# Performance work log

Hardware: AMD Instinct MI355X
Metric: run time of the kernel (lower is better)

The kernel has to match this reference:

```python
import jax, jax.numpy as jnp
import numpy as np
from jax import lax

NUM_HEADS = 8
EMBED_DIM = 256
KEY_DIM = EMBED_DIM // NUM_HEADS  # 32


def rotate_every_two(x):
    x1 = x[..., ::2]
    x2 = x[..., 1::2]
    return jnp.stack((-x2, x1), axis=-1).reshape(x.shape)


def theta_shift(x, sin, cos):
    return x * cos + rotate_every_two(x) * sin


def setup_inputs() -> dict:
    key = jax.random.key(0)
    ks = jax.random.split(key, 16)
    b, H, W, E = 16, 64, 64, EMBED_DIM
    kd = KEY_DIM
    gain = 2 ** (-2.5)
    std_proj = gain * (2.0 / (E + E)) ** 0.5  # xavier_normal with gain
    std_out = (2.0 / (E + E)) ** 0.5
    return {
        "x": jax.random.normal(ks[0], (b, H, W, E), jnp.float32),
        "sin": jax.random.normal(ks[1], (H, W, kd), jnp.float32),
        "cos": jax.random.normal(ks[2], (H, W, kd), jnp.float32),
        "mask_h": jax.random.normal(ks[3], (NUM_HEADS, H, H), jnp.float32),
        "mask_w": jax.random.normal(ks[4], (NUM_HEADS, W, W), jnp.float32),
        "q_w": jax.random.normal(ks[5], (E, E), jnp.float32) * std_proj,
        "q_b": jnp.zeros((E,), jnp.float32),
        "k_w": jax.random.normal(ks[6], (E, E), jnp.float32) * std_proj,
        "k_b": jnp.zeros((E,), jnp.float32),
        "v_w": jax.random.normal(ks[7], (E, E), jnp.float32) * std_proj,
        "v_b": jnp.zeros((E,), jnp.float32),
        "lepe_w": jax.random.normal(ks[8], (5, 5, 1, E), jnp.float32) * 0.05,  # HWIO depthwise
        "lepe_b": jnp.zeros((E,), jnp.float32),
        "out_w": jax.random.normal(ks[9], (E, E), jnp.float32) * std_out,
        "out_b": jnp.zeros((E,), jnp.float32),
    }


def reference(x, sin, cos, mask_h, mask_w, q_w, q_b, k_w, k_b, v_w, v_b,
              lepe_w, lepe_b, out_w, out_b):
    b, H, W, E = x.shape
    nH, kd = NUM_HEADS, KEY_DIM
    vd = E // nH
    scaling = kd ** (-0.5)

    q = x @ q_w + q_b                       # [b,H,W,E]
    k = (x @ k_w + k_b) * scaling
    v = x @ v_w + v_b

    # depthwise 5x5 conv (lepe), NHWC
    lepe = lax.conv_general_dilated(
        v, lepe_w, window_strides=(1, 1), padding=[(2, 2), (2, 2)],
        dimension_numbers=("NHWC", "HWIO", "NHWC"), feature_group_count=E) + lepe_b

    q = q.reshape(b, H, W, nH, kd)
    k = k.reshape(b, H, W, nH, kd)
    v = v.reshape(b, H, W, nH, vd)

    sin_b = sin[:, :, None, :]              # [H,W,1,kd]
    cos_b = cos[:, :, None, :]
    qr = theta_shift(q, sin_b, cos_b)       # [b,H,W,nH,kd]
    kr = theta_shift(k, sin_b, cos_b)

    # width-wise attention: scores [b,H,nH,W,W]
    qk_w = jnp.einsum("bhqnd,bhknd->bhnqk", qr, kr)
    attn_w = jax.nn.softmax(qk_w + mask_w[None, None], axis=-1)
    v1 = jnp.einsum("bhnqk,bhknd->bhqnd", attn_w, v)  # [b,H,W,nH,vd]

    # height-wise attention: scores [b,W,nH,H,H]
    qk_h = jnp.einsum("bqwnd,bkwnd->bwnqk", qr, kr)
    attn_h = jax.nn.softmax(qk_h + mask_h[None, None], axis=-1)
    out = jnp.einsum("bwnqk,bkwnd->bqwnd", attn_h, v1)  # [b,H,W,nH,vd]

    out = out.reshape(b, H, W, E) + lepe
    return out @ out_w + out_b
```

## Files before the change

### kernel.cpp

```cpp
#include <hip/hip_runtime.h>

typedef unsigned short u16;
typedef __attribute__((ext_vector_type(4))) float f32x4;
typedef __attribute__((ext_vector_type(8))) short bf16x8;
typedef __attribute__((ext_vector_type(8))) u16 u16x8;
typedef __attribute__((ext_vector_type(4))) u16 u16x4v;

#define DI __device__ __forceinline__

DI u16 f2bf(float f) {
  unsigned int x = __float_as_uint(f);
  unsigned int r = (x + 0x7fffu + ((x >> 16) & 1u)) >> 16;
  return (u16)r;
}
DI float bf2f(u16 u) { return __uint_as_float(((unsigned int)u) << 16); }

__global__ __launch_bounds__(256) void pack_kernel(
    const float* __restrict__ qw, const float* __restrict__ qb,
    const float* __restrict__ kw, const float* __restrict__ kb,
    const float* __restrict__ vw, const float* __restrict__ vb,
    const float* __restrict__ ow,
    u16* __restrict__ wqkvT, float* __restrict__ bias, u16* __restrict__ owT)
{
  const int r = blockIdx.x;
  const int t = threadIdx.x;
  if (r < 768) {
    const int p = r >> 8, c = r & 255;
    const float* wsrc = p == 0 ? qw : (p == 1 ? kw : vw);
    const float sc = (p == 1) ? 0.17677669529663687f : 1.0f;
    wqkvT[r * 256 + t] = f2bf(wsrc[t * 256 + c] * sc);
    if (t == 0) {
      const float* bs = p == 0 ? qb : (p == 1 ? kb : vb);
      bias[r] = bs[c] * sc;
    }
  } else {
    const int c = r - 768;
    owT[c * 256 + t] = f2bf(ow[t * 256 + c]);
  }
}

__global__ __launch_bounds__(256) void convert_kernel(
    const float* __restrict__ x, u16* __restrict__ xb)
{
  const int idx = blockIdx.x * 256 + threadIdx.x;
  const int tile = idx >> 12;
  const int within = idx & 4095;
  const int r = within >> 5;
  const int bc = (within & 31) << 4;
  const int sbc = bc ^ ((r & 7) << 4);
  const int row = (tile << 7) + r;
  const float* sp = x + row * 256 + (sbc >> 1);
  const float4 a = *reinterpret_cast<const float4*>(sp);
  const float4 b = *reinterpret_cast<const float4*>(sp + 4);
  u16x8 o;
  o[0] = f2bf(a.x); o[1] = f2bf(a.y); o[2] = f2bf(a.z); o[3] = f2bf(a.w);
  o[4] = f2bf(b.x); o[5] = f2bf(b.y); o[6] = f2bf(b.z); o[7] = f2bf(b.w);
  *reinterpret_cast<u16x8*>(xb + (idx << 3)) = o;
}

__global__ __launch_bounds__(256, 2) void qkv_gemm_kernel(
    const u16* __restrict__ xb, const u16* __restrict__ wT, const float* __restrict__ bias,
    const float* __restrict__ sinp, const float* __restrict__ cosp,
    u16* __restrict__ qr, u16* __restrict__ kr, u16* __restrict__ v)
{
  __shared__ u16 As[32768];
  __shared__ float Tr[4][1024];
  const int t = threadIdx.x;
  const int wave = t >> 6, lane = t & 63;
  const int g = lane >> 4, lr = lane & 15;
  const int wr = wave >> 1, wc = wave & 1;
  const int m0 = blockIdx.x * 128;

  {
    const u16* src = xb + (size_t)blockIdx.x * 32768;
    auto gsrc = (const __attribute__((address_space(1))) u16*)src;
    auto lds = (__attribute__((address_space(3))) u16*)As;
#pragma unroll
    for (int i = 0; i < 16; ++i) {
      const int o = wave * 8192 + i * 512;
      __builtin_amdgcn_global_load_lds(
          (const __attribute__((address_space(1))) void*)(gsrc + o + lane * 8),
          (__attribute__((address_space(3))) void*)(lds + o), 16, 0, 0);
    }
  }
  __syncthreads();

  const char* Ab = (const char*)As;
  float* Trw = Tr[wave];
  const int tl = (lane >> 3);
  const int cg8 = (lane & 7) * 8;

  for (int cg = 0; cg < 6; ++cg) {
    const int c0 = cg * 128;
    f32x4 acc[4][4];
#pragma unroll
    for (int i = 0; i < 4; ++i)
#pragma unroll
      for (int j = 0; j < 4; ++j) acc[i][j] = (f32x4){0.f, 0.f, 0.f, 0.f};

#pragma unroll
    for (int ks = 0; ks < 8; ++ks) {
      bf16x8 af[4], bfr[4];
#pragma unroll
      for (int mt = 0; mt < 4; ++mt) {
        const int rr = wr * 64 + mt * 16 + lr;
        const int cb = (ks * 64 + g * 16) ^ ((rr & 7) << 4);
        af[mt] = *reinterpret_cast<const bf16x8*>(Ab + rr * 512 + cb);
      }
#pragma unroll
      for (int nt = 0; nt < 4; ++nt)
        bfr[nt] = *reinterpret_cast<const bf16x8*>(wT + (c0 + wc * 64 + nt * 16 + lr) * 256 + ks * 32 + g * 8);
#pragma unroll
      for (int mt = 0; mt < 4; ++mt)
#pragma unroll
        for (int nt = 0; nt < 4; ++nt)
          acc[mt][nt] = __builtin_amdgcn_mfma_f32_16x16x32_bf16(af[mt], bfr[nt], acc[mt][nt], 0, 0, 0);
    }

    const int colb = c0 + wc * 64;
    const int proj = colb >> 8;
    u16* dst = proj == 0 ? qr : (proj == 1 ? kr : v);
    const int e0 = (colb & 255) + cg8;

    float bcv[4];
#pragma unroll
    for (int nt = 0; nt < 4; ++nt) bcv[nt] = bias[colb + nt * 16 + lr];

#pragma unroll
    for (int mt = 0; mt < 4; ++mt) {
#pragma unroll
      for (int nt = 0; nt < 4; ++nt)
#pragma unroll
        for (int j = 0; j < 4; ++j)
          Trw[(g * 4 + j) * 64 + ((nt * 16 + lr) ^ (g << 4))] = acc[mt][nt][j] + bcv[nt];
      asm volatile("s_waitcnt lgkmcnt(0)" ::: "memory");
#pragma unroll
      for (int r2 = 0; r2 < 2; ++r2) {
        const int row = tl + 8 * r2;
        const int rb = row * 64 + (cg8 ^ ((row >> 2) << 4));
        const float4 v0 = *reinterpret_cast<const float4*>(Trw + rb);
        const float4 v1 = *reinterpret_cast<const float4*>(Trw + rb + 4);
        const int tok = m0 + wr * 64 + mt * 16 + row;
        float r0, r1, r2v, r3, r4, r5, r6, r7;
        if (proj < 2) {
          const int pos = tok & 4095;
          const int d0 = cg8 & 31;
          const float* sp2 = sinp + pos * 32 + d0;
          const float* cp2 = cosp + pos * 32 + d0;
          const float4 s0 = *reinterpret_cast<const float4*>(sp2);
          const float4 s1 = *reinterpret_cast<const float4*>(sp2 + 4);
          const float4 cA = *reinterpret_cast<const float4*>(cp2);
          const float4 cB = *reinterpret_cast<const float4*>(cp2 + 4);
          r0  = v0.x * cA.x - v0.y * s0.x;
          r1  = v0.y * cA.y + v0.x * s0.y;
          r2v = v0.z * cA.z - v0.w * s0.z;
          r3  = v0.w * cA.w + v0.z * s0.w;
          r4  = v1.x * cB.x - v1.y * s1.x;
          r5  = v1.y * cB.y + v1.x * s1.y;
          r6  = v1.z * cB.z - v1.w * s1.z;
          r7  = v1.w * cB.w + v1.z * s1.w;
        } else {
          r0 = v0.x; r1 = v0.y; r2v = v0.z; r3 = v0.w;
          r4 = v1.x; r5 = v1.y; r6 = v1.z; r7 = v1.w;
        }
        u16x8 o;
        o[0] = f2bf(r0);  o[1] = f2bf(r1);  o[2] = f2bf(r2v); o[3] = f2bf(r3);
        o[4] = f2bf(r4);  o[5] = f2bf(r5);  o[6] = f2bf(r6);  o[7] = f2bf(r7);
        *reinterpret_cast<u16x8*>(dst + tok * 256 + e0) = o;
      }
      asm volatile("s_waitcnt lgkmcnt(0)" ::: "memory");
    }
  }
}

__global__ __launch_bounds__(256, 2) void attn_kernel(
    const u16* __restrict__ qr, const u16* __restrict__ kr, const u16* __restrict__ vsrc,
    const float* __restrict__ mask, u16* __restrict__ dst, const int mode)
{
  __shared__ u16 Pbuf[4][64][72];
  __shared__ u16 Vs[64][260];
  const int t = threadIdx.x;
  const int wave = t >> 6, lane = t & 63;
  const int g = lane >> 4, lr = lane & 15;
  const int b = blockIdx.x >> 6, o = blockIdx.x & 63;
  const int base = (mode == 0) ? (b * 4096 + o * 64) * 256 : (b * 4096 + o) * 256;
  const int ts = (mode == 0) ? 256 : 16384;

#pragma unroll
  for (int i = 0; i < 16; ++i) {
    const int idx = t + 256 * i;
    const int tok = idx >> 6, c4 = (idx & 63) << 2;
    *reinterpret_cast<u16x4v*>(&Vs[tok][c4]) =
        *reinterpret_cast<const u16x4v*>(vsrc + base + tok * ts + c4);
  }
  __syncthreads();

  for (int hh = 0; hh < 2; ++hh) {
    const int n = wave * 2 + hh;
    bf16x8 qf[4], kf[4];
#pragma unroll
    for (int mt = 0; mt < 4; ++mt) {
      qf[mt] = *reinterpret_cast<const bf16x8*>(qr + base + (mt * 16 + lr) * ts + n * 32 + g * 8);
      kf[mt] = *reinterpret_cast<const bf16x8*>(kr + base + (mt * 16 + lr) * ts + n * 32 + g * 8);
    }
    const f32x4 zero = (f32x4){0.f, 0.f, 0.f, 0.f};
    f32x4 s[4][4];
#pragma unroll
    for (int mt = 0; mt < 4; ++mt)
#pragma unroll
      for (int nt = 0; nt < 4; ++nt)
        s[mt][nt] = __builtin_amdgcn_mfma_f32_16x16x32_bf16(qf[mt], kf[nt], zero, 0, 0, 0);

    const float* mp = mask + n * 4096;
#pragma unroll
    for (int mt = 0; mt < 4; ++mt) {
#pragma unroll
      for (int j = 0; j < 4; ++j) {
        const int r = mt * 16 + g * 4 + j;
#pragma unroll
        for (int nt = 0; nt < 4; ++nt)
          s[mt][nt][j] += mp[r * 64 + nt * 16 + lr];
        float m = fmaxf(fmaxf(s[mt][0][j], s[mt][1][j]), fmaxf(s[mt][2][j], s[mt][3][j]));
        m = fmaxf(m, __shfl_xor(m, 1));
        m = fmaxf(m, __shfl_xor(m, 2));
        m = fmaxf(m, __shfl_xor(m, 4));
        m = fmaxf(m, __shfl_xor(m, 8));
        float sum = 0.f;
#pragma unroll
        for (int nt = 0; nt < 4; ++nt) {
          const float p = __expf(s[mt][nt][j] - m);
          s[mt][nt][j] = p;
          sum += p;
        }
        sum += __shfl_xor(sum, 1);
        sum += __shfl_xor(sum, 2);
        sum += __shfl_xor(sum, 4);
        sum += __shfl_xor(sum, 8);
        const float rs = 1.f / sum;
#pragma unroll
        for (int nt = 0; nt < 4; ++nt)
          Pbuf[wave][r][nt * 16 + lr] = f2bf(s[mt][nt][j] * rs);
      }
    }
    __syncthreads();

    f32x4 oacc[4][2];
#pragma unroll
    for (int mt = 0; mt < 4; ++mt)
#pragma unroll
      for (int nd = 0; nd < 2; ++nd) oacc[mt][nd] = zero;

#pragma unroll
    for (int kt = 0; kt < 2; ++kt) {
      bf16x8 pa[4];
#pragma unroll
      for (int mt = 0; mt < 4; ++mt)
        pa[mt] = *reinterpret_cast<const bf16x8*>(&Pbuf[wave][mt * 16 + lr][kt * 32 + g * 8]);
#pragma unroll
      for (int nd = 0; nd < 2; ++nd) {
        const int dcol = n * 32 + nd * 16 + lr;
        bf16x8 vb;
#pragma unroll
        for (int j2 = 0; j2 < 8; ++j2)
          vb[j2] = (short)Vs[kt * 32 + g * 8 + j2][dcol];
#pragma unroll
        for (int mt = 0; mt < 4; ++mt)
          oacc[mt][nd] = __builtin_amdgcn_mfma_f32_16x16x32_bf16(pa[mt], vb, oacc[mt][nd], 0, 0, 0);
      }
    }
#pragma unroll
    for (int mt = 0; mt < 4; ++mt)
#pragma unroll
      for (int nd = 0; nd < 2; ++nd)
#pragma unroll
        for (int j = 0; j < 4; ++j)
          dst[base + (mt * 16 + g * 4 + j) * ts + n * 32 + nd * 16 + lr] = f2bf(oacc[mt][nd][j]);
    __syncthreads();
  }
}

__global__ __launch_bounds__(256) void lepe_kernel(
    const u16* __restrict__ v, const float* __restrict__ cw, const float* __restrict__ cb,
    u16* __restrict__ lepe)
{
  const int t = threadIdx.x;
  const int cg = t & 31, pg = t >> 5;
  const int c0 = cg * 8;
  const int rowi = blockIdx.x >> 1;
  const int w0 = (blockIdx.x & 1) * 32 + pg * 4;
  const int h = rowi & 63;

  float acc[4][8];
#pragma unroll
  for (int p = 0; p < 4; ++p)
#pragma unroll
    for (int j = 0; j < 8; ++j) acc[p][j] = 0.f;

#pragma unroll
  for (int dy = 0; dy < 5; ++dy) {
    const int hh = h + dy - 2;
    if ((unsigned)hh >= 64u) continue;
    const u16* vrow = v + (size_t)(rowi + dy - 2) * 64 * 256 + c0;
    float fin[8][8];
#pragma unroll
    for (int i = 0; i < 8; ++i) {
      const int ww = w0 - 2 + i;
      if ((unsigned)ww < 64u) {
        const u16x8 val = *reinterpret_cast<const u16x8*>(vrow + ww * 256);
#pragma unroll
        for (int j = 0; j < 8; ++j) fin[i][j] = bf2f(val[j]);
      } else {
#pragma unroll
        for (int j = 0; j < 8; ++j) fin[i][j] = 0.f;
      }
    }
#pragma unroll
    for (int dx = 0; dx < 5; ++dx) {
      const float* wp = cw + (dy * 5 + dx) * 256 + c0;
      const float4 wA = *reinterpret_cast<const float4*>(wp);
      const float4 wB = *reinterpret_cast<const float4*>(wp + 4);
      const float wv[8] = {wA.x, wA.y, wA.z, wA.w, wB.x, wB.y, wB.z, wB.w};
#pragma unroll
      for (int p = 0; p < 4; ++p)
#pragma unroll
        for (int j = 0; j < 8; ++j)
          acc[p][j] += fin[p + dx][j] * wv[j];
    }
  }

#pragma unroll
  for (int p = 0; p < 4; ++p) {
    u16x8 r;
#pragma unroll
    for (int j = 0; j < 8; ++j) r[j] = f2bf(acc[p][j] + cb[c0 + j]);
    *reinterpret_cast<u16x8*>(lepe + ((size_t)rowi * 64 + w0 + p) * 256 + c0) = r;
  }
}

__global__ __launch_bounds__(256, 2) void out_gemm_kernel(
    const u16* __restrict__ ao, const u16* __restrict__ lep, const u16* __restrict__ owT,
    const float* __restrict__ ob, float* __restrict__ out)
{
  __shared__ u16 As[32768];
  const int t = threadIdx.x;
  const int wave = t >> 6, lane = t & 63;
  const int g = lane >> 4, lr = lane & 15;
  const int wr = wave >> 1, wc = wave & 1;
  const int m0 = blockIdx.x * 128;

  char* Abw = (char*)As;
#pragma unroll
  for (int i = 0; i < 16; ++i) {
    const int idx = t + 256 * i;
    const int r = idx >> 5;
    const int bc = (idx & 31) << 4;
    const int off = (m0 + r) * 256 + (bc >> 1);
    const u16x8 a = *reinterpret_cast<const u16x8*>(ao + off);
    const u16x8 l = *reinterpret_cast<const u16x8*>(lep + off);
    u16x8 s;
#pragma unroll
    for (int j = 0; j < 8; ++j) s[j] = f2bf(bf2f(a[j]) + bf2f(l[j]));
    *reinterpret_cast<u16x8*>(Abw + r * 512 + (bc ^ ((r & 7) << 4))) = s;
  }
  __syncthreads();

  const char* Ab = (const char*)As;
  for (int cg = 0; cg < 2; ++cg) {
    const int c0 = cg * 128;
    f32x4 acc[4][4];
#pragma unroll
    for (int i = 0; i < 4; ++i)
#pragma unroll
      for (int j = 0; j < 4; ++j) acc[i][j] = (f32x4){0.f, 0.f, 0.f, 0.f};

#pragma unroll
    for (int ks = 0; ks < 8; ++ks) {
      bf16x8 af[4], bfr[4];
#pragma unroll
      for (int mt = 0; mt < 4; ++mt) {
        const int rr = wr * 64 + mt * 16 + lr;
        const int cb = (ks * 64 + g * 16) ^ ((rr & 7) << 4);
        af[mt] = *reinterpret_cast<const bf16x8*>(Ab + rr * 512 + cb);
      }
#pragma unroll
      for (int nt = 0; nt < 4; ++nt)
        bfr[nt] = *reinterpret_cast<const bf16x8*>(owT + (c0 + wc * 64 + nt * 16 + lr) * 256 + ks * 32 + g * 8);
#pragma unroll
      for (int mt = 0; mt < 4; ++mt)
#pragma unroll
        for (int nt = 0; nt < 4; ++nt)
          acc[mt][nt] = __builtin_amdgcn_mfma_f32_16x16x32_bf16(af[mt], bfr[nt], acc[mt][nt], 0, 0, 0);
    }

#pragma unroll
    for (int mt = 0; mt < 4; ++mt) {
#pragma unroll
      for (int nt = 0; nt < 4; ++nt) {
        const int col = c0 + wc * 64 + nt * 16 + lr;
        const float bc2 = ob[col];
#pragma unroll
        for (int j = 0; j < 4; ++j) {
          const int tok = m0 + wr * 64 + mt * 16 + g * 4 + j;
          out[tok * 256 + col] = acc[mt][nt][j] + bc2;
        }
      }
    }
  }
}

extern "C" void kernel_launch(void* const* d_in, const int* in_sizes, int n_in,
                              void* d_out, int out_size, void* d_ws, size_t ws_size,
                              hipStream_t stream)
{
  const float* x      = (const float*)d_in[0];
  const float* sinp   = (const float*)d_in[1];
  const float* cosp   = (const float*)d_in[2];
  const float* mask_h = (const float*)d_in[3];
  const float* mask_w = (const float*)d_in[4];
  const float* q_w    = (const float*)d_in[5];
  const float* q_b    = (const float*)d_in[6];
  const float* k_w    = (const float*)d_in[7];
  const float* k_b    = (const float*)d_in[8];
  const float* v_w    = (const float*)d_in[9];
  const float* v_b    = (const float*)d_in[10];
  const float* lepe_w = (const float*)d_in[11];
  const float* lepe_b = (const float*)d_in[12];
  const float* out_w  = (const float*)d_in[13];
  const float* out_b  = (const float*)d_in[14];

  unsigned char* ws = (unsigned char*)d_ws;
  const size_t SZ = 33554432;
  u16* qr    = (u16*)(ws);
  u16* kr    = (u16*)(ws + SZ);
  u16* vv    = (u16*)(ws + 2 * SZ);
  u16* v1    = (u16*)(ws + 3 * SZ);
  u16* xb    = (u16*)(ws + 4 * SZ);
  u16* lepe  = (u16*)(ws + 4 * SZ);
  u16* wqkvT = (u16*)(ws + 5 * SZ);
  u16* owT   = (u16*)(ws + 5 * SZ + 393216);
  float* bias = (float*)(ws + 5 * SZ + 393216 + 131072);
  u16* attn_out = vv;

  pack_kernel<<<1024, 256, 0, stream>>>(q_w, q_b, k_w, k_b, v_w, v_b, out_w, wqkvT, bias, owT);
  convert_kernel<<<8192, 256, 0, stream>>>(x, xb);
  qkv_gemm_kernel<<<512, 256, 0, stream>>>(xb, wqkvT, bias, sinp, cosp, qr, kr, vv);
  lepe_kernel<<<2048, 256, 0, stream>>>(vv, lepe_w, lepe_b, lepe);
  attn_kernel<<<1024, 256, 0, stream>>>(qr, kr, vv, mask_w, v1, 0);
  attn_kernel<<<1024, 256, 0, stream>>>(qr, kr, v1, mask_h, attn_out, 1);
  out_gemm_kernel<<<512, 256, 0, stream>>>(attn_out, lepe, owT, out_b, (float*)d_out);
}
```

Baseline: 281.8 us.

## Transpose V in LDS for vector MFMA loads and retile output GEMM

The attention kernel stores V transposed with an XOR swizzle in shared memory, so each lane loads the MFMA B operand with one 128-bit read instead of eight strided scalar reads. It also drops the per-head block barriers, since each wave only uses its own buffers. The output GEMM moves to 64-row tiles with each wave owning 32 columns, doubles the grid, and swaps the MFMA operands so results are written as contiguous float4 rows with vector bias loads. The V transpose uses scalar LDS writes during the load phase, and smaller GEMM tiles mean more reloads of the output weight.

```diff
diff --git a/kernel.cpp b/kernel.cpp
--- a/kernel.cpp
+++ b/kernel.cpp
@@ -178,7 +178,7 @@
     const float* __restrict__ mask, u16* __restrict__ dst, const int mode)
 {
   __shared__ u16 Pbuf[4][64][72];
-  __shared__ u16 Vs[64][260];
+  __shared__ u16 Vt[256][80];
   const int t = threadIdx.x;
   const int wave = t >> 6, lane = t & 63;
   const int g = lane >> 4, lr = lane & 15;
@@ -187,11 +187,13 @@
   const int ts = (mode == 0) ? 256 : 16384;
 
 #pragma unroll
-  for (int i = 0; i < 16; ++i) {
-    const int idx = t + 256 * i;
-    const int tok = idx >> 6, c4 = (idx & 63) << 2;
-    *reinterpret_cast<u16x4v*>(&Vs[tok][c4]) =
-        *reinterpret_cast<const u16x4v*>(vsrc + base + tok * ts + c4);
+  for (int i = 0; i < 8; ++i) {
+    const int c = t + 256 * i;
+    const int tok = c >> 5, ch = c & 31;
+    const u16x8 val = *reinterpret_cast<const u16x8*>(vsrc + base + tok * ts + ch * 8);
+    const int tc = tok ^ ((ch & 7) * 8);
+#pragma unroll
+    for (int j = 0; j < 8; ++j) Vt[ch * 8 + j][tc] = val[j];
   }
   __syncthreads();
 
@@ -242,7 +244,6 @@
           Pbuf[wave][r][nt * 16 + lr] = f2bf(s[mt][nt][j] * rs);
       }
     }
-    __syncthreads();
 
     f32x4 oacc[4][2];
 #pragma unroll
@@ -259,10 +260,8 @@
 #pragma unroll
       for (int nd = 0; nd < 2; ++nd) {
         const int dcol = n * 32 + nd * 16 + lr;
-        bf16x8 vb;
-#pragma unroll
-        for (int j2 = 0; j2 < 8; ++j2)
-          vb[j2] = (short)Vs[kt * 32 + g * 8 + j2][dcol];
+        const bf16x8 vb = *reinterpret_cast<const bf16x8*>(
+            &Vt[dcol][(kt * 32 + g * 8) ^ (((dcol >> 3) & 7) * 8)]);
 #pragma unroll
         for (int mt = 0; mt < 4; ++mt)
           oacc[mt][nd] = __builtin_amdgcn_mfma_f32_16x16x32_bf16(pa[mt], vb, oacc[mt][nd], 0, 0, 0);
@@ -275,7 +274,6 @@
 #pragma unroll
         for (int j = 0; j < 4; ++j)
           dst[base + (mt * 16 + g * 4 + j) * ts + n * 32 + nd * 16 + lr] = f2bf(oacc[mt][nd][j]);
-    __syncthreads();
   }
 }
 
@@ -337,72 +335,72 @@
   }
 }
 
-__global__ __launch_bounds__(256, 2) void out_gemm_kernel(
+__global__ __launch_bounds__(256, 4) void out_gemm_kernel(
     const u16* __restrict__ ao, const u16* __restrict__ lep, const u16* __restrict__ owT,
     const float* __restrict__ ob, float* __restrict__ out)
 {
-  __shared__ u16 As[32768];
+  __shared__ u16 As[16384];
   const int t = threadIdx.x;
   const int wave = t >> 6, lane = t & 63;
   const int g = lane >> 4, lr = lane & 15;
-  const int wr = wave >> 1, wc = wave & 1;
-  const int m0 = blockIdx.x * 128;
+  const int m0 = blockIdx.x * 64;
 
   char* Abw = (char*)As;
 #pragma unroll
-  for (int i = 0; i < 16; ++i) {
-    const int idx = t + 256 * i;
-    const int r = idx >> 5;
-    const int bc = (idx & 31) << 4;
-    const int off = (m0 + r) * 256 + (bc >> 1);
+  for (int i = 0; i < 8; ++i) {
+    const int c = t + 256 * i;
+    const int row = c >> 5, bc = (c & 31) << 4;
+    const int off = (m0 + row) * 256 + (c & 31) * 8;
     const u16x8 a = *reinterpret_cast<const u16x8*>(ao + off);
     const u16x8 l = *reinterpret_cast<const u16x8*>(lep + off);
     u16x8 s;
 #pragma unroll
     for (int j = 0; j < 8; ++j) s[j] = f2bf(bf2f(a[j]) + bf2f(l[j]));
-    *reinterpret_cast<u16x8*>(Abw + r * 512 + (bc ^ ((r & 7) << 4))) = s;
+    *reinterpret_cast<u16x8*>(Abw + row * 512 + (bc ^ ((row & 7) << 4))) = s;
   }
   __syncthreads();
 
   const char* Ab = (const char*)As;
   for (int cg = 0; cg < 2; ++cg) {
-    const int c0 = cg * 128;
-    f32x4 acc[4][4];
+    const int c0w = cg * 128 + wave * 32;
+    f32x4 acc[4][2];
 #pragma unroll
     for (int i = 0; i < 4; ++i)
 #pragma unroll
-      for (int j = 0; j < 4; ++j) acc[i][j] = (f32x4){0.f, 0.f, 0.f, 0.f};
+      for (int j = 0; j < 2; ++j) acc[i][j] = (f32x4){0.f, 0.f, 0.f, 0.f};
 
 #pragma unroll
     for (int ks = 0; ks < 8; ++ks) {
-      bf16x8 af[4], bfr[4];
+      bf16x8 af[4], bfr[2];
 #pragma unroll
       for (int mt = 0; mt < 4; ++mt) {
-        const int rr = wr * 64 + mt * 16 + lr;
+        const int rr = mt * 16 + lr;
         const int cb = (ks * 64 + g * 16) ^ ((rr & 7) << 4);
         af[mt] = *reinterpret_cast<const bf16x8*>(Ab + rr * 512 + cb);
       }
 #pragma unroll
-      for (int nt = 0; nt < 4; ++nt)
-        bfr[nt] = *reinterpret_cast<const bf16x8*>(owT + (c0 + wc * 64 + nt * 16 + lr) * 256 + ks * 32 + g * 8);
+      for (int nt = 0; nt < 2; ++nt)
+        bfr[nt] = *reinterpret_cast<const bf16x8*>(owT + (c0w + nt * 16 + lr) * 256 + ks * 32 + g * 8);
 #pragma unroll
       for (int mt = 0; mt < 4; ++mt)
 #pragma unroll
-        for (int nt = 0; nt < 4; ++nt)
-          acc[mt][nt] = __builtin_amdgcn_mfma_f32_16x16x32_bf16(af[mt], bfr[nt], acc[mt][nt], 0, 0, 0);
+        for (int nt = 0; nt < 2; ++nt)
+          acc[mt][nt] = __builtin_amdgcn_mfma_f32_16x16x32_bf16(bfr[nt], af[mt], acc[mt][nt], 0, 0, 0);
     }
 
 #pragma unroll
     for (int mt = 0; mt < 4; ++mt) {
-#pragma unroll
-      for (int nt = 0; nt < 4; ++nt) {
-        const int col = c0 + wc * 64 + nt * 16 + lr;
-        const float bc2 = ob[col];
-#pragma unroll
-        for (int j = 0; j < 4; ++j) {
-          const int tok = m0 + wr * 64 + mt * 16 + g * 4 + j;
-          out[tok * 256 + col] = acc[mt][nt][j] + bc2;
-        }
+      const int tok = m0 + mt * 16 + lr;
+#pragma unroll
+      for (int nt = 0; nt < 2; ++nt) {
+        const int col0 = c0w + nt * 16 + g * 4;
+        const float4 ob4 = *reinterpret_cast<const float4*>(ob + col0);
+        float4 o;
+        o.x = acc[mt][nt][0] + ob4.x;
+        o.y = acc[mt][nt][1] + ob4.y;
+        o.z = acc[mt][nt][2] + ob4.z;
+        o.w = acc[mt][nt][3] + ob4.w;
+        *reinterpret_cast<float4*>(out + tok * 256 + col0) = o;
       }
     }
   }
@@ -447,5 +445,5 @@
   lepe_kernel<<<2048, 256, 0, stream>>>(vv, lepe_w, lepe_b, lepe);
   attn_kernel<<<1024, 256, 0, stream>>>(qr, kr, vv, mask_w, v1, 0);
   attn_kernel<<<1024, 256, 0, stream>>>(qr, kr, v1, mask_h, attn_out, 1);
-  out_gemm_kernel<<<512, 256, 0, stream>>>(attn_out, lepe, owT, out_b, (float*)d_out);
-}
+  out_gemm_kernel<<<1024, 256, 0, stream>>>(attn_out, lepe, owT, out_b, (float*)d_out);
+}
```

Measured after the change: 276.0 us. 1.02x faster.
